# Optimization experiments

Measured on AMD Instinct MI355X. Metric: run time of the kernel, lower is better.

Reference implementation:

```python
import jax, jax.numpy as jnp
import numpy as np

B, S, D = 2, 2048, 2048
H, KVH, HD = 16, 4, 128
NREP = H // KVH  # GQA repeat factor


def _rope(x, cos, sin):
    # x: [B,S,h,HD]; pairs (x[2k], x[2k+1]) form complex numbers
    xr = x[..., 0::2]
    xi = x[..., 1::2]
    cos = cos[None, :, None, :]  # [1,S,1,HD/2]
    sin = sin[None, :, None, :]
    out_r = xr * cos - xi * sin
    out_i = xr * sin + xi * cos
    return jnp.stack([out_r, out_i], axis=-1).reshape(x.shape)


def setup_inputs() -> dict:
    key = jax.random.key(0)
    ks = jax.random.split(key, 5)
    x = jax.random.normal(ks[0], (B, S, D), dtype=jnp.float32)
    # standard rotary frequencies
    inv_freq = 1.0 / (10000.0 ** (np.arange(0, HD, 2, dtype=np.float64) / HD))
    ang = np.outer(np.arange(S, dtype=np.float64), inv_freq)
    freqs_cos = jnp.asarray(np.cos(ang), dtype=jnp.float32)  # [S, HD/2]
    freqs_sin = jnp.asarray(np.sin(ang), dtype=jnp.float32)
    wq = jax.random.normal(ks[1], (D, H * HD), dtype=jnp.float32) * 0.02
    wk = jax.random.normal(ks[2], (D, KVH * HD), dtype=jnp.float32) * 0.02
    wv = jax.random.normal(ks[3], (D, KVH * HD), dtype=jnp.float32) * 0.02
    wo = jax.random.normal(ks[4], (H * HD, D), dtype=jnp.float32) * 0.02
    cache_k = jnp.zeros((B, S, KVH, HD), dtype=jnp.float32)
    cache_v = jnp.zeros((B, S, KVH, HD), dtype=jnp.float32)
    return {"x": x, "freqs_cos": freqs_cos, "freqs_sin": freqs_sin,
            "wq": wq, "wk": wk, "wv": wv, "wo": wo,
            "cache_k": cache_k, "cache_v": cache_v, "start_pos": 0}


def reference(x, freqs_cos, freqs_sin, wq, wk, wv, wo, cache_k, cache_v, start_pos):
    b, s, _ = x.shape
    xq = (x @ wq).reshape(b, s, H, HD)
    xk = (x @ wk).reshape(b, s, KVH, HD)
    xv = (x @ wv).reshape(b, s, KVH, HD)
    xq = _rope(xq, freqs_cos, freqs_sin)
    xk = _rope(xk, freqs_cos, freqs_sin)
    # KV cache update + slice (start_pos is a static Python int)
    ck = cache_k.at[:, start_pos:start_pos + s].set(xk)
    cv = cache_v.at[:, start_pos:start_pos + s].set(xv)
    keys = ck[:, :start_pos + s]    # [B,T,KVH,HD]
    vals = cv[:, :start_pos + s]
    # GQA without materializing repeat_kv: group query heads per kv head
    q = xq.reshape(b, s, KVH, NREP, HD)
    scores = jnp.einsum('bsknd,btkd->bknst', q, keys) / np.float32(np.sqrt(HD))
    probs = jax.nn.softmax(scores.astype(jnp.float32), axis=-1).astype(x.dtype)
    out = jnp.einsum('bknst,btkd->bsknd', probs, vals).reshape(b, s, H * HD)
    return out @ wo
```

## Files before the change

### kernel.cpp

```cpp
#include <hip/hip_runtime.h>
#include <stdint.h>
#include <stddef.h>

#define S_LEN  2048
#define NH     16
#define NKVH   4
#define HD_    128
#define DMODEL 2048
#define NQKV   3072
#define MROWS  4096

typedef __attribute__((ext_vector_type(8)))  __bf16 bf16x8;
typedef __attribute__((ext_vector_type(4)))  __bf16 bf16x4;
typedef __attribute__((ext_vector_type(4)))  float  f32x4;
typedef __attribute__((ext_vector_type(16))) float  f32x16;

#define MFMA16(a, b, c) __builtin_amdgcn_mfma_f32_16x16x32_bf16((a), (b), (c), 0, 0, 0)
#define MFMA32(a, b, c) __builtin_amdgcn_mfma_f32_32x32x16_bf16((a), (b), (c), 0, 0, 0)

__device__ __forceinline__ void gload16(const void* g, void* l) {
  __builtin_amdgcn_global_load_lds((const __attribute__((address_space(1))) void*)g,
                                   (__attribute__((address_space(3))) void*)l,
                                   16, 0, 0);
}

__device__ __forceinline__ uint32_t cvtpk(float lo, float hi) {
  uint32_t d;
  asm("v_cvt_pk_bf16_f32 %0, %1, %2" : "=v"(d) : "v"(lo), "v"(hi));
  return d;
}
__device__ __forceinline__ void pswap(uint32_t& a, uint32_t& b) {
  asm("s_nop 1\n\tv_permlane32_swap_b32 %0, %1" : "+v"(a), "+v"(b));
}
__device__ __forceinline__ float fast_exp2(float x) {
  float r;
  asm("v_exp_f32 %0, %1\n\ts_nop 0" : "=v"(r) : "v"(x));
  return r;
}

__global__ void prep_kernel(const float* __restrict__ x, __bf16* __restrict__ xb,
                            const float* __restrict__ wq, const float* __restrict__ wk,
                            const float* __restrict__ wv, const float* __restrict__ wo,
                            __bf16* __restrict__ wqkvT, __bf16* __restrict__ woT) {
  __shared__ float tile[64][65];
  const int bid = blockIdx.x;
  const int tid = threadIdx.x;
  if (bid < 8192) {
    size_t i = (size_t)bid * 256 + tid;
    const float4* xv = (const float4*)x;
    float4 v = xv[i];
    bf16x4 o;
    o[0] = (__bf16)v.x; o[1] = (__bf16)v.y; o[2] = (__bf16)v.z; o[3] = (__bf16)v.w;
    *(bf16x4*)(xb + i * 4) = o;
    return;
  }
  int b2 = bid - 8192;
  const float* W; __bf16* WT; int ldw, kx, ny;
  if (b2 < 1024)      { W = wq; WT = wqkvT;                        ldw = 2048; kx = b2 & 31; ny = b2 >> 5; }
  else if (b2 < 1280) { int t = b2 - 1024; W = wk; WT = wqkvT + (size_t)2048 * 2048; ldw = 512; kx = t & 31; ny = t >> 5; }
  else if (b2 < 1536) { int t = b2 - 1280; W = wv; WT = wqkvT + (size_t)2560 * 2048; ldw = 512; kx = t & 31; ny = t >> 5; }
  else                { int t = b2 - 1536; W = wo; WT = woT;       ldw = 2048; kx = t & 31; ny = t >> 5; }
  const int k0 = kx * 64, n0 = ny * 64;
#pragma unroll
  for (int r = 0; r < 16; ++r) {
    int idx = r * 256 + tid;
    int kr = idx >> 6, nc = idx & 63;
    tile[kr][nc] = W[(size_t)(k0 + kr) * ldw + n0 + nc];
  }
  __syncthreads();
#pragma unroll
  for (int r = 0; r < 16; ++r) {
    int idx = r * 256 + tid;
    int nr = idx >> 6, kc = idx & 63;
    WT[(size_t)(n0 + nr) * 2048 + k0 + kc] = (__bf16)tile[kc][nr];
  }
}

template <int MODE>
__global__ __launch_bounds__(256, 2) void gemm_kernel(
    const __bf16* __restrict__ A, int lda,
    const __bf16* __restrict__ Bt, int ldb,
    void* __restrict__ Cout, int ldc, int Kdim,
    const float* __restrict__ fc, const float* __restrict__ fs,
    __bf16* __restrict__ xq, __bf16* __restrict__ Kp, __bf16* __restrict__ VTp) {
  __shared__ __attribute__((aligned(16))) __bf16 As[128 * 64];
  __shared__ __attribute__((aligned(16))) __bf16 Bs[128 * 64];
  const int tid = threadIdx.x;
  const int w = tid >> 6, l = tid & 63, lg = l >> 4, lr = l & 15;
  const int wm = w >> 1, wn = w & 1;

  const int nwg = gridDim.x * gridDim.y;
  const int lid = blockIdx.y * gridDim.x + blockIdx.x;
  const int swz = (lid & 7) * (nwg >> 3) + (lid >> 3);
  const int bx = swz % gridDim.x, by = swz / gridDim.x;
  const int m0 = by * 128, n0 = bx * 128;

  f32x4 acc[4][4] = {};

  for (int k0 = 0; k0 < Kdim; k0 += 64) {
#pragma unroll
    for (int t = 0; t < 4; ++t) {
      int o = (t * 256 + tid) * 16;
      int row = o >> 7;
      int slot = (o >> 4) & 7;
      int sw = slot ^ (row & 7);
      gload16(A + (size_t)(m0 + row) * lda + k0 + sw * 8,
              (char*)As + t * 4096 + (w << 10));
      gload16(Bt + (size_t)(n0 + row) * ldb + k0 + sw * 8,
              (char*)Bs + t * 4096 + (w << 10));
    }
    __syncthreads();
#pragma unroll
    for (int c = 0; c < 2; ++c) {
      bf16x8 af[4];
#pragma unroll
      for (int mi = 0; mi < 4; ++mi) {
        int row = wm * 64 + mi * 16 + lr;
        int slot = (c * 4 + lg) ^ (row & 7);
        af[mi] = *(const bf16x8*)((const char*)As + row * 128 + slot * 16);
      }
#pragma unroll
      for (int ni = 0; ni < 4; ++ni) {
        int rn = wn * 64 + ni * 16 + lr;
        int slot = (c * 4 + lg) ^ (rn & 7);
        bf16x8 bfr = *(const bf16x8*)((const char*)Bs + rn * 128 + slot * 16);
#pragma unroll
        for (int mi = 0; mi < 4; ++mi)
          acc[mi][ni] = MFMA16(af[mi], bfr, acc[mi][ni]);
      }
    }
    __syncthreads();
  }

  if (MODE == 1) {
    const float qs = 0.12755102871936672f;
    if (n0 < 2560) {
#pragma unroll
      for (int mi = 0; mi < 4; ++mi)
#pragma unroll
        for (int ni = 0; ni < 4; ++ni)
#pragma unroll
          for (int i = 0; i < 4; ++i) {
            float v = acc[mi][ni][i];
            float p = __shfl_xor(v, 1);
            int cc = n0 + wn * 64 + ni * 16 + lr;
            int r  = m0 + wm * 64 + mi * 16 + lg * 4 + i;
            int s  = r & (S_LEN - 1);
            int j  = (cc & 127) >> 1;
            float c = fc[s * 64 + j], sn = fs[s * 64 + j];
            float o = (lr & 1) ? (p * sn + v * c)
                               : (v * c - p * sn);
            if (n0 < DMODEL) {
              xq[(size_t)r * DMODEL + cc] = (__bf16)(o * qs);
            } else {
              int bb = r >> 11, kt = s >> 6, rr = s & 63;
              int kvh = (cc - DMODEL) >> 7, dk = (cc - DMODEL) & 127;
              size_t e = ((size_t)((bb * 4 + kvh) * 32 + kt) * 16 + (dk >> 3)) * 512
                         + rr * 8 + (dk & 7);
              Kp[e] = (__bf16)o;
            }
          }
    } else {
#pragma unroll
      for (int mi = 0; mi < 4; ++mi)
#pragma unroll
        for (int ni = 0; ni < 4; ++ni)
#pragma unroll
          for (int i = 0; i < 4; ++i) {
            float v = acc[mi][ni][i];
            int cc = n0 + wn * 64 + ni * 16 + lr;
            int r  = m0 + wm * 64 + mi * 16 + lg * 4 + i;
            int s  = r & (S_LEN - 1);
            int bb = r >> 11, kt = s >> 6, rr = s & 63;
            int kvh = (cc - 2560) >> 7, d = (cc - 2560) & 127;
            size_t e = ((size_t)((bb * 4 + kvh) * 32 + kt) * 8 + (rr >> 3)) * 1024
                       + d * 8 + (rr & 7);
            VTp[e] = (__bf16)v;
          }
    }
    return;
  }

#pragma unroll
  for (int mi = 0; mi < 4; ++mi)
#pragma unroll
    for (int ni = 0; ni < 4; ++ni)
#pragma unroll
      for (int i = 0; i < 4; ++i) {
        int r = m0 + wm * 64 + mi * 16 + lg * 4 + i;
        int cc = n0 + wn * 64 + ni * 16 + lr;
        ((float*)Cout)[(size_t)r * ldc + cc] = acc[mi][ni][i];
      }
}

__global__ __launch_bounds__(256, 2) void attn_kernel(
    const __bf16* __restrict__ xq, const __bf16* __restrict__ Kp,
    const __bf16* __restrict__ VTp, __bf16* __restrict__ out) {
  __shared__ __attribute__((aligned(16))) __bf16 Ks0[64 * 128];
  __shared__ __attribute__((aligned(16))) __bf16 Ks1[64 * 128];
  __shared__ __attribute__((aligned(16))) __bf16 Vs0[128 * 64];
  __shared__ __attribute__((aligned(16))) __bf16 Vs1[128 * 64];
  const int tid = threadIdx.x;
  const int w = tid >> 6, l = tid & 63;
  const int qc = l & 31, hi = l >> 5;
  const int bh = blockIdx.y;
  const int b = bh >> 4, h = bh & 15, kvh = h >> 2;
  const int bkv = b * NKVH + kvh;
  const int q0 = blockIdx.x * 128 + w * 32;

  const __bf16* Ktiles = Kp  + (size_t)bkv * 32 * 8192;
  const __bf16* Vtiles = VTp + (size_t)bkv * 32 * 8192;

  auto stage = [&](int kt, __bf16* ksb, __bf16* vsb) {
    const __bf16* ksrc = Ktiles + (size_t)kt * 8192;
    const __bf16* vsrc = Vtiles + (size_t)kt * 8192;
#pragma unroll
    for (int t = 0; t < 4; ++t) {
      gload16(ksrc + (t * 256 + tid) * 8, (char*)ksb + t * 4096 + (w << 10));
      gload16(vsrc + (t * 256 + tid) * 8, (char*)vsb + t * 4096 + (w << 10));
    }
  };

  bf16x8 aq[8];
#pragma unroll
  for (int c = 0; c < 8; ++c)
    aq[c] = *(const bf16x8*)(xq + (size_t)(b * S_LEN + q0 + qc) * DMODEL +
                             h * HD_ + c * 16 + hi * 8);

  f32x16 o_acc[4] = {};
  float m = -1e30f, lsum = 0.0f;

  typedef union { uint32_t u[4]; bf16x8 v; } pfrag_t;

  auto tile_step = [&](const __bf16* ksb, const __bf16* vsb) {
    const char* kb = (const char*)ksb + hi * 1024 + qc * 16;
    const char* vb = (const char*)vsb + hi * 2048 + qc * 16;

    f32x16 st[2] = {};
    __builtin_amdgcn_s_setprio(1);
#pragma unroll
    for (int t = 0; t < 2; ++t) {
#pragma unroll
      for (int c = 0; c < 8; ++c) {
        bf16x8 kf = *(const bf16x8*)(kb + c * 2048 + t * 512);
        st[t] = MFMA32(kf, aq[c], st[t]);
      }
    }
    __builtin_amdgcn_s_setprio(0);

    float pm = st[0][0];
#pragma unroll
    for (int t = 0; t < 2; ++t)
#pragma unroll
      for (int r = 0; r < 16; ++r) pm = fmaxf(pm, st[t][r]);
    pm = fmaxf(pm, __shfl_xor(pm, 32));

    if (__any(pm - m > 11.54f)) {
      float mn = fmaxf(m, pm);
      float sf = fast_exp2(m - mn);
      lsum *= sf;
#pragma unroll
      for (int dt = 0; dt < 4; ++dt)
#pragma unroll
        for (int r = 0; r < 16; ++r) o_acc[dt][r] *= sf;
      m = mn;
    }

    float rsum = 0.0f;
#pragma unroll
    for (int t = 0; t < 2; ++t)
#pragma unroll
      for (int r = 0; r < 16; ++r) {
        st[t][r] = fast_exp2(st[t][r] - m);
        rsum += st[t][r];
      }
    rsum += __shfl_xor(rsum, 32);
    lsum += rsum;

    pfrag_t pf[4];
#pragma unroll
    for (int t = 0; t < 2; ++t)
#pragma unroll
      for (int half = 0; half < 2; ++half) {
        int bs = half * 8;
        uint32_t x0 = cvtpk(st[t][bs + 0], st[t][bs + 1]);
        uint32_t y0 = cvtpk(st[t][bs + 4], st[t][bs + 5]);
        uint32_t x1 = cvtpk(st[t][bs + 2], st[t][bs + 3]);
        uint32_t y1 = cvtpk(st[t][bs + 6], st[t][bs + 7]);
        pswap(x0, y0);
        pswap(x1, y1);
        pf[t * 2 + half].u[0] = x0;
        pf[t * 2 + half].u[1] = x1;
        pf[t * 2 + half].u[2] = y0;
        pf[t * 2 + half].u[3] = y1;
      }

    __builtin_amdgcn_s_setprio(1);
#pragma unroll
    for (int dt = 0; dt < 4; ++dt) {
#pragma unroll
      for (int ks = 0; ks < 4; ++ks) {
        bf16x8 vf = *(const bf16x8*)(vb + ks * 4096 + dt * 512);
        o_acc[dt] = MFMA32(vf, pf[ks].v, o_acc[dt]);
      }
    }
    __builtin_amdgcn_s_setprio(0);
  };

  stage(0, Ks0, Vs0);
  __syncthreads();

#pragma unroll 1
  for (int kt = 0; kt < S_LEN / 64; kt += 2) {
    stage(kt + 1, Ks1, Vs1);
    tile_step(Ks0, Vs0);
    __syncthreads();
    if (kt + 2 < S_LEN / 64) stage(kt + 2, Ks0, Vs0);
    tile_step(Ks1, Vs1);
    __syncthreads();
  }

  float rinv = 1.0f / lsum;
  const size_t orow = (size_t)(b * S_LEN + q0 + qc) * DMODEL + h * HD_;
#pragma unroll
  for (int dt = 0; dt < 4; ++dt)
#pragma unroll
    for (int rg = 0; rg < 4; ++rg) {
      bf16x4 ov;
#pragma unroll
      for (int i = 0; i < 4; ++i)
        ov[i] = (__bf16)(o_acc[dt][rg * 4 + i] * rinv);
      int d = dt * 32 + rg * 8 + hi * 4;
      *(bf16x4*)(out + orow + d) = ov;
    }
}

extern "C" void kernel_launch(void* const* d_in, const int* in_sizes, int n_in,
                              void* d_out, int out_size, void* d_ws, size_t ws_size,
                              hipStream_t stream) {
  const float* x  = (const float*)d_in[0];
  const float* fc = (const float*)d_in[1];
  const float* fs = (const float*)d_in[2];
  const float* wq = (const float*)d_in[3];
  const float* wk = (const float*)d_in[4];
  const float* wv = (const float*)d_in[5];
  const float* wo = (const float*)d_in[6];

  char* ws = (char*)d_ws;
  __bf16* xb    = (__bf16*)(ws);
  __bf16* wqkvT = (__bf16*)(ws + (16u << 20));
  __bf16* woT   = (__bf16*)(ws + (28u << 20));
  __bf16* xq    = (__bf16*)(ws + (36u << 20));
  __bf16* Kp    = (__bf16*)(ws + (52u << 20));
  __bf16* VTp   = (__bf16*)(ws + (56u << 20));

  prep_kernel<<<10752, 256, 0, stream>>>(x, xb, wq, wk, wv, wo, wqkvT, woT);
  {
    dim3 g(NQKV / 128, MROWS / 128);
    gemm_kernel<1><<<g, 256, 0, stream>>>(xb, 2048, wqkvT, 2048, nullptr, 0, 2048,
                                          fc, fs, xq, Kp, VTp);
  }
  {
    dim3 g(S_LEN / 128, 32);
    attn_kernel<<<g, 256, 0, stream>>>(xq, Kp, VTp, xb);
  }
  {
    dim3 g(DMODEL / 128, MROWS / 128);
    gemm_kernel<0><<<g, 256, 0, stream>>>(xb, 2048, woT, 2048, d_out, 2048, 2048,
                                          fc, fs, nullptr, nullptr, nullptr);
  }
}
```

Before: 194.2 us.

## Split attention KV range across two blocks and merge with combine kernel

Attention is split along the key dimension into two halves via a third grid dimension, doubling the block count from 512 to 1024. Each block writes a partial bf16 output plus its running max and sum, and a new combine kernel merges the halves into the final output. The double-buffered LDS staging is replaced by a single buffer with a sync before and after each tile, so global loads no longer overlap compute. This adds an extra kernel launch, extra partial-output traffic through d_out scratch, and an extra bf16 rounding of the partials.

```diff
diff --git a/kernel.cpp b/kernel.cpp
--- a/kernel.cpp
+++ b/kernel.cpp
@@ -36,6 +36,15 @@
   float r;
   asm("v_exp_f32 %0, %1\n\ts_nop 0" : "=v"(r) : "v"(x));
   return r;
+}
+__device__ __forceinline__ float bf2f(uint16_t u) {
+  uint32_t x = ((uint32_t)u) << 16;
+  return __builtin_bit_cast(float, x);
+}
+__device__ __forceinline__ uint16_t f2bf(float f) {
+  uint32_t u = __builtin_bit_cast(uint32_t, f);
+  uint32_t r = (u + 0x7FFFu + ((u >> 16) & 1u)) >> 16;
+  return (uint16_t)r;
 }
 
 __global__ void prep_kernel(const float* __restrict__ x, __bf16* __restrict__ xb,
@@ -195,29 +204,30 @@
 
 __global__ __launch_bounds__(256, 2) void attn_kernel(
     const __bf16* __restrict__ xq, const __bf16* __restrict__ Kp,
-    const __bf16* __restrict__ VTp, __bf16* __restrict__ out) {
-  __shared__ __attribute__((aligned(16))) __bf16 Ks0[64 * 128];
-  __shared__ __attribute__((aligned(16))) __bf16 Ks1[64 * 128];
-  __shared__ __attribute__((aligned(16))) __bf16 Vs0[128 * 64];
-  __shared__ __attribute__((aligned(16))) __bf16 Vs1[128 * 64];
+    const __bf16* __restrict__ VTp, __bf16* __restrict__ out0,
+    __bf16* __restrict__ out1, float2* __restrict__ ml) {
+  __shared__ __attribute__((aligned(16))) __bf16 Ks[64 * 128];
+  __shared__ __attribute__((aligned(16))) __bf16 Vs[128 * 64];
   const int tid = threadIdx.x;
   const int w = tid >> 6, l = tid & 63;
   const int qc = l & 31, hi = l >> 5;
   const int bh = blockIdx.y;
+  const int half = blockIdx.z;
   const int b = bh >> 4, h = bh & 15, kvh = h >> 2;
   const int bkv = b * NKVH + kvh;
   const int q0 = blockIdx.x * 128 + w * 32;
+  const int kt0 = half * 16;
 
   const __bf16* Ktiles = Kp  + (size_t)bkv * 32 * 8192;
   const __bf16* Vtiles = VTp + (size_t)bkv * 32 * 8192;
 
-  auto stage = [&](int kt, __bf16* ksb, __bf16* vsb) {
+  auto stage = [&](int kt) {
     const __bf16* ksrc = Ktiles + (size_t)kt * 8192;
     const __bf16* vsrc = Vtiles + (size_t)kt * 8192;
 #pragma unroll
     for (int t = 0; t < 4; ++t) {
-      gload16(ksrc + (t * 256 + tid) * 8, (char*)ksb + t * 4096 + (w << 10));
-      gload16(vsrc + (t * 256 + tid) * 8, (char*)vsb + t * 4096 + (w << 10));
+      gload16(ksrc + (t * 256 + tid) * 8, (char*)Ks + t * 4096 + (w << 10));
+      gload16(vsrc + (t * 256 + tid) * 8, (char*)Vs + t * 4096 + (w << 10));
     }
   };
 
@@ -232,9 +242,9 @@
 
   typedef union { uint32_t u[4]; bf16x8 v; } pfrag_t;
 
-  auto tile_step = [&](const __bf16* ksb, const __bf16* vsb) {
-    const char* kb = (const char*)ksb + hi * 1024 + qc * 16;
-    const char* vb = (const char*)vsb + hi * 2048 + qc * 16;
+  auto tile_step = [&]() {
+    const char* kb = (const char*)Ks + hi * 1024 + qc * 16;
+    const char* vb = (const char*)Vs + hi * 2048 + qc * 16;
 
     f32x16 st[2] = {};
     __builtin_amdgcn_s_setprio(1);
@@ -281,18 +291,18 @@
 #pragma unroll
     for (int t = 0; t < 2; ++t)
 #pragma unroll
-      for (int half = 0; half < 2; ++half) {
-        int bs = half * 8;
+      for (int half2 = 0; half2 < 2; ++half2) {
+        int bs = half2 * 8;
         uint32_t x0 = cvtpk(st[t][bs + 0], st[t][bs + 1]);
         uint32_t y0 = cvtpk(st[t][bs + 4], st[t][bs + 5]);
         uint32_t x1 = cvtpk(st[t][bs + 2], st[t][bs + 3]);
         uint32_t y1 = cvtpk(st[t][bs + 6], st[t][bs + 7]);
         pswap(x0, y0);
         pswap(x1, y1);
-        pf[t * 2 + half].u[0] = x0;
-        pf[t * 2 + half].u[1] = x1;
-        pf[t * 2 + half].u[2] = y0;
-        pf[t * 2 + half].u[3] = y1;
+        pf[t * 2 + half2].u[0] = x0;
+        pf[t * 2 + half2].u[1] = x1;
+        pf[t * 2 + half2].u[2] = y0;
+        pf[t * 2 + half2].u[3] = y1;
       }
 
     __builtin_amdgcn_s_setprio(1);
@@ -307,21 +317,18 @@
     __builtin_amdgcn_s_setprio(0);
   };
 
-  stage(0, Ks0, Vs0);
-  __syncthreads();
-
 #pragma unroll 1
-  for (int kt = 0; kt < S_LEN / 64; kt += 2) {
-    stage(kt + 1, Ks1, Vs1);
-    tile_step(Ks0, Vs0);
+  for (int t = 0; t < 16; ++t) {
+    stage(kt0 + t);
     __syncthreads();
-    if (kt + 2 < S_LEN / 64) stage(kt + 2, Ks0, Vs0);
-    tile_step(Ks1, Vs1);
+    tile_step();
     __syncthreads();
   }
 
+  __bf16* outp = half ? out1 : out0;
   float rinv = 1.0f / lsum;
-  const size_t orow = (size_t)(b * S_LEN + q0 + qc) * DMODEL + h * HD_;
+  const int row = b * S_LEN + q0 + qc;
+  const size_t orow = (size_t)row * DMODEL + h * HD_;
 #pragma unroll
   for (int dt = 0; dt < 4; ++dt)
 #pragma unroll
@@ -331,8 +338,35 @@
       for (int i = 0; i < 4; ++i)
         ov[i] = (__bf16)(o_acc[dt][rg * 4 + i] * rinv);
       int d = dt * 32 + rg * 8 + hi * 4;
-      *(bf16x4*)(out + orow + d) = ov;
-    }
+      *(bf16x4*)(outp + orow + d) = ov;
+    }
+  if (hi == 0) {
+    float2 v; v.x = m; v.y = lsum;
+    ml[(size_t)half * (MROWS * NH) + (size_t)row * NH + h] = v;
+  }
+}
+
+__global__ void combine_kernel(__bf16* __restrict__ out0,
+                               const __bf16* __restrict__ out1,
+                               const float2* __restrict__ ml) {
+  const int tid = threadIdx.x;
+  const int unit = blockIdx.x * 4 + (tid >> 6);
+  const int lane = tid & 63;
+  const int row = unit >> 4, h = unit & 15;
+  float2 ml0 = ml[(size_t)row * NH + h];
+  float2 ml1 = ml[(size_t)(MROWS * NH) + (size_t)row * NH + h];
+  float M = fmaxf(ml0.x, ml1.x);
+  float w0 = fast_exp2(ml0.x - M) * ml0.y;
+  float w1 = fast_exp2(ml1.x - M) * ml1.y;
+  float inv = 1.0f / (w0 + w1);
+  w0 *= inv; w1 *= inv;
+  size_t e = (size_t)row * DMODEL + h * HD_ + lane * 2;
+  uint32_t a = *(const uint32_t*)(out0 + e);
+  uint32_t c = *(const uint32_t*)(out1 + e);
+  float lo = w0 * bf2f((uint16_t)(a & 0xFFFFu)) + w1 * bf2f((uint16_t)(c & 0xFFFFu));
+  float hi2 = w0 * bf2f((uint16_t)(a >> 16)) + w1 * bf2f((uint16_t)(c >> 16));
+  uint32_t r = (uint32_t)f2bf(lo) | ((uint32_t)f2bf(hi2) << 16);
+  *(uint32_t*)(out0 + e) = r;
 }
 
 extern "C" void kernel_launch(void* const* d_in, const int* in_sizes, int n_in,
@@ -353,6 +387,8 @@
   __bf16* xq    = (__bf16*)(ws + (36u << 20));
   __bf16* Kp    = (__bf16*)(ws + (52u << 20));
   __bf16* VTp   = (__bf16*)(ws + (56u << 20));
+  __bf16* o1 = (__bf16*)d_out;
+  float2* ml = (float2*)((char*)d_out + (16u << 20));
 
   prep_kernel<<<10752, 256, 0, stream>>>(x, xb, wq, wk, wv, wo, wqkvT, woT);
   {
@@ -361,9 +397,10 @@
                                           fc, fs, xq, Kp, VTp);
   }
   {
-    dim3 g(S_LEN / 128, 32);
-    attn_kernel<<<g, 256, 0, stream>>>(xq, Kp, VTp, xb);
-  }
+    dim3 g(S_LEN / 128, 32, 2);
+    attn_kernel<<<g, 256, 0, stream>>>(xq, Kp, VTp, xb, o1, ml);
+  }
+  combine_kernel<<<16384, 256, 0, stream>>>(xb, o1, ml);
   {
     dim3 g(DMODEL / 128, MROWS / 128);
     gemm_kernel<0><<<g, 256, 0, stream>>>(xb, 2048, woT, 2048, d_out, 2048, 2048,
```

Result: slower. 212.4 us (+9.4%).
